# Performance work log

Measured on AMD Instinct MI355X. Metric: run time of the kernel, lower is better.

The kernel has to match this reference:

```python
import jax, jax.numpy as jnp
import numpy as np

DIM = 128
B = 262144


def setup_inputs() -> dict:
    key = jax.random.key(0)
    k_t, k_w1, k_b1, k_w2, k_b2 = jax.random.split(key, 5)
    t = jax.random.uniform(k_t, (B,), dtype=jnp.float32)  # t in [0, 1]
    s = 1.0 / np.sqrt(DIM)  # torch Linear default init scale
    W1 = jax.random.uniform(k_w1, (DIM, DIM), dtype=jnp.float32, minval=-s, maxval=s)
    b1 = jax.random.uniform(k_b1, (DIM,), dtype=jnp.float32, minval=-s, maxval=s)
    W2 = jax.random.uniform(k_w2, (DIM, DIM), dtype=jnp.float32, minval=-s, maxval=s)
    b2 = jax.random.uniform(k_b2, (DIM,), dtype=jnp.float32, minval=-s, maxval=s)
    return {"t": t, "W1": W1, "b1": b1, "W2": W2, "b2": b2}


def reference(t, W1, b1, W2, b2):
    # create_timestep_embedding, vectorized over batch and dim:
    #   emb[b, i] = t[b]*cos(i/dim*pi*t[b]) + t[b]*sin(i/dim*pi*(1 - t[b]))
    phase = (jnp.arange(DIM, dtype=t.dtype) / DIM) * jnp.pi  # [DIM]
    tb = t[:, None]  # [B, 1]
    emb = tb * jnp.cos(phase[None, :] * tb) + tb * jnp.sin(phase[None, :] * (1.0 - tb))  # [B, DIM]
    x = jax.nn.silu(emb @ W1.T + b1)  # Linear128 + SiLU
    x = jax.nn.silu(x @ W2.T + b2)    # Linear128 + SiLU
    return x
```

## Files before the change

### kernel.cpp

```cpp
#include <hip/hip_runtime.h>

typedef _Float16 f16;
typedef _Float16 f16x2 __attribute__((ext_vector_type(2)));
typedef _Float16 f16x8 __attribute__((ext_vector_type(8)));
typedef float    f32x4 __attribute__((ext_vector_type(4)));

#define DIM 128

__device__ __forceinline__ float silu_f(float x) {
    float e = __builtin_amdgcn_exp2f(x * -1.44269504088896341f);
    return x * __builtin_amdgcn_rcpf(1.0f + e);
}

__global__ __launch_bounds__(256, 2)
void ts_mlp_kernel(const float* __restrict__ t,
                   const float* __restrict__ W1, const float* __restrict__ b1,
                   const float* __restrict__ W2, const float* __restrict__ b2,
                   float* __restrict__ out, int B) {
    __shared__ f16x8 w1f[4][8][64];
    __shared__ f16x8 w2f[4][8][64];
    __shared__ f16x2 x1p[4][256][4];

    const int tid  = threadIdx.x;
    const int wv   = tid >> 6;
    const int lane = tid & 63;
    const int q    = lane >> 4;
    const int ln   = lane & 15;
    const int par  = lane & 1;

    for (int mtx = 0; mtx < 2; ++mtx) {
        const float* W = mtx ? W2 : W1;
        for (int nti = 0; nti < 2; ++nti) {
            const int nt = wv * 2 + nti;
            const int n  = nt * 16 + ln;
            for (int kt = 0; kt < 4; ++kt) {
                const int k0 = kt * 32 + q * 8;
                const float4* src = (const float4*)(W + n * DIM + k0);
                float4 lo = src[0], hi = src[1];
                f16x8 fr;
                fr[0] = (f16)lo.x; fr[1] = (f16)lo.y; fr[2] = (f16)lo.z; fr[3] = (f16)lo.w;
                fr[4] = (f16)hi.x; fr[5] = (f16)hi.y; fr[6] = (f16)hi.z; fr[7] = (f16)hi.w;
                if (mtx) w2f[kt][nt][lane] = fr; else w1f[kt][nt][lane] = fr;
            }
        }
    }
    float b1v[8], b2v[8];
#pragma unroll
    for (int nt = 0; nt < 8; ++nt) {
        b1v[nt] = b1[nt * 16 + ln];
        b2v[nt] = b2[nt * 16 + ln];
    }
    __syncthreads();

    const int ntiles = B >> 6;
    for (int tile = blockIdx.x; tile < ntiles; tile += gridDim.x) {
        const int row0 = tile * 64 + wv * 16;

        const float tv   = t[row0 + ln];
        const float t256 = tv * 0.00390625f;
        const float o256 = (1.0f - tv) * 0.00390625f;
        f16x8 af[4];
#pragma unroll
        for (int kt = 0; kt < 4; ++kt) {
#pragma unroll
            for (int j = 0; j < 8; ++j) {
                const float fd = (float)(kt * 32 + q * 8 + j);
                const float c  = __builtin_amdgcn_cosf(fd * t256);
                const float s  = __builtin_amdgcn_sinf(fd * o256);
                af[kt][j] = (f16)(tv * (c + s));
            }
        }

        f32x4 acc[8];
#pragma unroll
        for (int nt = 0; nt < 8; ++nt) acc[nt] = (f32x4){0.f, 0.f, 0.f, 0.f};
#pragma unroll
        for (int kt = 0; kt < 4; ++kt) {
#pragma unroll
            for (int nt = 0; nt < 8; ++nt) {
                acc[nt] = __builtin_amdgcn_mfma_f32_16x16x32_f16(
                    af[kt], w1f[kt][nt][lane], acc[nt], 0, 0, 0);
            }
        }

#pragma unroll
        for (int nt = 0; nt < 8; ++nt) {
            float v[4], pv[4];
#pragma unroll
            for (int r = 0; r < 4; ++r) v[r] = silu_f(acc[nt][r] + b1v[nt]);
#pragma unroll
            for (int r = 0; r < 4; ++r) pv[r] = __shfl_xor(v[r], 1, 64);
            const int k0  = nt * 16 + (ln & 14);
            const int cch = k0 >> 3;
            const int hw  = (k0 & 7) >> 1;
#pragma unroll
            for (int p = 0; p < 2; ++p) {
                const int r = par * 2 + p;
                const int m = q * 4 + r;
                const float lo = par ? pv[r] : v[r];
                const float hi = par ? v[r] : pv[r];
                f16x2 h; h.x = (f16)lo; h.y = (f16)hi;
                x1p[wv][m * 16 + (cch ^ m)][hw] = h;
            }
        }

        f32x4 acc2[8];
#pragma unroll
        for (int nt = 0; nt < 8; ++nt) acc2[nt] = (f32x4){0.f, 0.f, 0.f, 0.f};
#pragma unroll
        for (int kt = 0; kt < 4; ++kt) {
            const f16x8 a2 = *(const f16x8*)&x1p[wv][ln * 16 + ((kt * 4 + q) ^ ln)][0];
#pragma unroll
            for (int nt = 0; nt < 8; ++nt) {
                acc2[nt] = __builtin_amdgcn_mfma_f32_16x16x32_f16(
                    a2, w2f[kt][nt][lane], acc2[nt], 0, 0, 0);
            }
        }

#pragma unroll
        for (int nt = 0; nt < 8; ++nt) {
#pragma unroll
            for (int r = 0; r < 4; ++r) {
                const float o = silu_f(acc2[nt][r] + b2v[nt]);
                out[(size_t)(row0 + q * 4 + r) * DIM + nt * 16 + ln] = o;
            }
        }
    }
}

extern "C" void kernel_launch(void* const* d_in, const int* in_sizes, int n_in,
                              void* d_out, int out_size, void* d_ws, size_t ws_size,
                              hipStream_t stream) {
    const float* t  = (const float*)d_in[0];
    const float* W1 = (const float*)d_in[1];
    const float* b1 = (const float*)d_in[2];
    const float* W2 = (const float*)d_in[3];
    const float* b2 = (const float*)d_in[4];
    float* out = (float*)d_out;
    const int B = in_sizes[0];
    const int ntiles = B >> 6;
    int grid = ntiles < 512 ? ntiles : 512;
    ts_mlp_kernel<<<dim3(grid), dim3(256), 0, stream>>>(t, W1, b1, W2, b2, out, B);
}
```

Measured before the change: 192.0 us.

## Keep weight fragments in registers and split waves over output columns

Each wave now holds its 32-column slice of W1 and W2 as f16 MFMA fragments in registers. Previously every wave read all weights from LDS on every tile. The embedding tile and the layer-1 activations are shared across waves through LDS, which adds two block barriers per tile. The next tile's t values are prefetched, and the occupancy hint and grid size are raised to three blocks per CU. The aim is to cut per-tile LDS weight traffic, at the cost of extra synchronisation and higher register pressure.

Measured after the change: 194.3 us. Within noise of the previous version (+1.2%).

```diff
diff --git a/kernel.cpp b/kernel.cpp
--- a/kernel.cpp
+++ b/kernel.cpp
@@ -12,14 +12,13 @@
     return x * __builtin_amdgcn_rcpf(1.0f + e);
 }
 
-__global__ __launch_bounds__(256, 2)
+__global__ __launch_bounds__(256, 3)
 void ts_mlp_kernel(const float* __restrict__ t,
                    const float* __restrict__ W1, const float* __restrict__ b1,
                    const float* __restrict__ W2, const float* __restrict__ b2,
                    float* __restrict__ out, int B) {
-    __shared__ f16x8 w1f[4][8][64];
-    __shared__ f16x8 w2f[4][8][64];
-    __shared__ f16x2 x1p[4][256][4];
+    __shared__ f16x8 embs[4][4][64];
+    __shared__ f16x2 x1s[4][256][4];
 
     const int tid  = threadIdx.x;
     const int wv   = tid >> 6;
@@ -28,101 +27,127 @@
     const int ln   = lane & 15;
     const int par  = lane & 1;
 
-    for (int mtx = 0; mtx < 2; ++mtx) {
-        const float* W = mtx ? W2 : W1;
-        for (int nti = 0; nti < 2; ++nti) {
-            const int nt = wv * 2 + nti;
-            const int n  = nt * 16 + ln;
-            for (int kt = 0; kt < 4; ++kt) {
-                const int k0 = kt * 32 + q * 8;
-                const float4* src = (const float4*)(W + n * DIM + k0);
-                float4 lo = src[0], hi = src[1];
-                f16x8 fr;
-                fr[0] = (f16)lo.x; fr[1] = (f16)lo.y; fr[2] = (f16)lo.z; fr[3] = (f16)lo.w;
-                fr[4] = (f16)hi.x; fr[5] = (f16)hi.y; fr[6] = (f16)hi.z; fr[7] = (f16)hi.w;
-                if (mtx) w2f[kt][nt][lane] = fr; else w1f[kt][nt][lane] = fr;
-            }
+    f16x8 w1r[2][4], w2r[2][4];
+#pragma unroll
+    for (int nl = 0; nl < 2; ++nl) {
+        const int n = wv * 32 + nl * 16 + ln;
+#pragma unroll
+        for (int kt = 0; kt < 4; ++kt) {
+            const int k0 = kt * 32 + q * 8;
+            const float4* s1 = (const float4*)(W1 + n * DIM + k0);
+            float4 lo = s1[0], hi = s1[1];
+            f16x8 fr;
+            fr[0] = (f16)lo.x; fr[1] = (f16)lo.y; fr[2] = (f16)lo.z; fr[3] = (f16)lo.w;
+            fr[4] = (f16)hi.x; fr[5] = (f16)hi.y; fr[6] = (f16)hi.z; fr[7] = (f16)hi.w;
+            w1r[nl][kt] = fr;
+            const float4* s2 = (const float4*)(W2 + n * DIM + k0);
+            lo = s2[0]; hi = s2[1];
+            fr[0] = (f16)lo.x; fr[1] = (f16)lo.y; fr[2] = (f16)lo.z; fr[3] = (f16)lo.w;
+            fr[4] = (f16)hi.x; fr[5] = (f16)hi.y; fr[6] = (f16)hi.z; fr[7] = (f16)hi.w;
+            w2r[nl][kt] = fr;
         }
     }
-    float b1v[8], b2v[8];
+    float b1v[2], b2v[2];
 #pragma unroll
-    for (int nt = 0; nt < 8; ++nt) {
-        b1v[nt] = b1[nt * 16 + ln];
-        b2v[nt] = b2[nt * 16 + ln];
+    for (int nl = 0; nl < 2; ++nl) {
+        b1v[nl] = b1[wv * 32 + nl * 16 + ln];
+        b2v[nl] = b2[wv * 32 + nl * 16 + ln];
     }
-    __syncthreads();
 
     const int ntiles = B >> 6;
-    for (int tile = blockIdx.x; tile < ntiles; tile += gridDim.x) {
-        const int row0 = tile * 64 + wv * 16;
+    int tile = blockIdx.x;
+    float tv_next = (tile < ntiles) ? t[tile * 64 + wv * 16 + ln] : 0.0f;
 
-        const float tv   = t[row0 + ln];
+    for (; tile < ntiles; tile += gridDim.x) {
+        const float tv = tv_next;
+        const int nxt = tile + gridDim.x;
+        if (nxt < ntiles) tv_next = t[nxt * 64 + wv * 16 + ln];
+
         const float t256 = tv * 0.00390625f;
         const float o256 = (1.0f - tv) * 0.00390625f;
-        f16x8 af[4];
 #pragma unroll
         for (int kt = 0; kt < 4; ++kt) {
+            f16x8 fr;
 #pragma unroll
             for (int j = 0; j < 8; ++j) {
                 const float fd = (float)(kt * 32 + q * 8 + j);
                 const float c  = __builtin_amdgcn_cosf(fd * t256);
                 const float s  = __builtin_amdgcn_sinf(fd * o256);
-                af[kt][j] = (f16)(tv * (c + s));
+                fr[j] = (f16)(tv * (c + s));
             }
+            embs[wv][kt][lane] = fr;
         }
+        __syncthreads();
 
-        f32x4 acc[8];
+        f32x4 acc[4][2];
 #pragma unroll
-        for (int nt = 0; nt < 8; ++nt) acc[nt] = (f32x4){0.f, 0.f, 0.f, 0.f};
+        for (int g = 0; g < 4; ++g)
 #pragma unroll
-        for (int kt = 0; kt < 4; ++kt) {
+            for (int nl = 0; nl < 2; ++nl) acc[g][nl] = (f32x4){0.f, 0.f, 0.f, 0.f};
 #pragma unroll
-            for (int nt = 0; nt < 8; ++nt) {
-                acc[nt] = __builtin_amdgcn_mfma_f32_16x16x32_f16(
-                    af[kt], w1f[kt][nt][lane], acc[nt], 0, 0, 0);
+        for (int g = 0; g < 4; ++g) {
+#pragma unroll
+            for (int kt = 0; kt < 4; ++kt) {
+                const f16x8 a = embs[g][kt][lane];
+#pragma unroll
+                for (int nl = 0; nl < 2; ++nl)
+                    acc[g][nl] = __builtin_amdgcn_mfma_f32_16x16x32_f16(
+                        a, w1r[nl][kt], acc[g][nl], 0, 0, 0);
             }
         }
 
 #pragma unroll
-        for (int nt = 0; nt < 8; ++nt) {
-            float v[4], pv[4];
+        for (int g = 0; g < 4; ++g) {
 #pragma unroll
-            for (int r = 0; r < 4; ++r) v[r] = silu_f(acc[nt][r] + b1v[nt]);
+            for (int nl = 0; nl < 2; ++nl) {
+                float v[4], pv[4];
 #pragma unroll
-            for (int r = 0; r < 4; ++r) pv[r] = __shfl_xor(v[r], 1, 64);
-            const int k0  = nt * 16 + (ln & 14);
-            const int cch = k0 >> 3;
-            const int hw  = (k0 & 7) >> 1;
+                for (int r = 0; r < 4; ++r) v[r] = silu_f(acc[g][nl][r] + b1v[nl]);
 #pragma unroll
-            for (int p = 0; p < 2; ++p) {
-                const int r = par * 2 + p;
-                const int m = q * 4 + r;
-                const float lo = par ? pv[r] : v[r];
-                const float hi = par ? v[r] : pv[r];
-                f16x2 h; h.x = (f16)lo; h.y = (f16)hi;
-                x1p[wv][m * 16 + (cch ^ m)][hw] = h;
+                for (int r = 0; r < 4; ++r) pv[r] = __shfl_xor(v[r], 1, 64);
+                const int col = wv * 32 + nl * 16 + (ln & 14);
+                const int cch = col >> 3;
+                const int hw  = (col & 7) >> 1;
+#pragma unroll
+                for (int p = 0; p < 2; ++p) {
+                    const int r = par * 2 + p;
+                    const int m = q * 4 + r;
+                    const float lo = par ? pv[r] : v[r];
+                    const float hi = par ? v[r] : pv[r];
+                    f16x2 h; h.x = (f16)lo; h.y = (f16)hi;
+                    x1s[g][m * 16 + (cch ^ m)][hw] = h;
+                }
             }
         }
+        __syncthreads();
 
-        f32x4 acc2[8];
+        f32x4 acc2[4][2];
 #pragma unroll
-        for (int nt = 0; nt < 8; ++nt) acc2[nt] = (f32x4){0.f, 0.f, 0.f, 0.f};
+        for (int g = 0; g < 4; ++g)
 #pragma unroll
-        for (int kt = 0; kt < 4; ++kt) {
-            const f16x8 a2 = *(const f16x8*)&x1p[wv][ln * 16 + ((kt * 4 + q) ^ ln)][0];
+            for (int nl = 0; nl < 2; ++nl) acc2[g][nl] = (f32x4){0.f, 0.f, 0.f, 0.f};
 #pragma unroll
-            for (int nt = 0; nt < 8; ++nt) {
-                acc2[nt] = __builtin_amdgcn_mfma_f32_16x16x32_f16(
-                    a2, w2f[kt][nt][lane], acc2[nt], 0, 0, 0);
+        for (int g = 0; g < 4; ++g) {
+#pragma unroll
+            for (int kt = 0; kt < 4; ++kt) {
+                const f16x8 a2 = *(const f16x8*)&x1s[g][ln * 16 + ((kt * 4 + q) ^ ln)][0];
+#pragma unroll
+                for (int nl = 0; nl < 2; ++nl)
+                    acc2[g][nl] = __builtin_amdgcn_mfma_f32_16x16x32_f16(
+                        a2, w2r[nl][kt], acc2[g][nl], 0, 0, 0);
             }
         }
 
 #pragma unroll
-        for (int nt = 0; nt < 8; ++nt) {
+        for (int g = 0; g < 4; ++g) {
 #pragma unroll
-            for (int r = 0; r < 4; ++r) {
-                const float o = silu_f(acc2[nt][r] + b2v[nt]);
-                out[(size_t)(row0 + q * 4 + r) * DIM + nt * 16 + ln] = o;
+            for (int nl = 0; nl < 2; ++nl) {
+#pragma unroll
+                for (int r = 0; r < 4; ++r) {
+                    const float o = silu_f(acc2[g][nl][r] + b2v[nl]);
+                    out[(size_t)(tile * 64 + g * 16 + q * 4 + r) * DIM
+                        + wv * 32 + nl * 16 + ln] = o;
+                }
             }
         }
     }
@@ -139,6 +164,6 @@
     float* out = (float*)d_out;
     const int B = in_sizes[0];
     const int ntiles = B >> 6;
-    int grid = ntiles < 512 ? ntiles : 512;
+    int grid = ntiles < 768 ? ntiles : 768;
     ts_mlp_kernel<<<dim3(grid), dim3(256), 0, stream>>>(t, W1, b1, W2, b2, out, B);
 }
```
